# Kernel tuning notes

Measured on AMD Instinct MI355X. Metric: run time of the kernel, lower is better.

Reference implementation:

```python
import jax, jax.numpy as jnp
import numpy as np

BINS = np.array([1, 2, 3, 4, 8, 16, 32, 64], dtype=np.int32)


def setup_inputs() -> dict:
    N, G, F, H, K = 1024, 620, 20, 150, 128
    D_in = 3 * G + F  # 1880
    key = jax.random.key(0)
    ks = jax.random.split(key, 10)
    g = jax.random.normal(ks[0], (N, G), dtype=jnp.float32)
    si = jax.random.normal(ks[1], (N,), dtype=jnp.float32)
    i1 = jnp.sort(jax.random.randint(ks[2], (N,), 0, 8192)).astype(jnp.int32)
    i2 = jnp.sort(jax.random.randint(ks[3], (N,), 0, 8192)).astype(jnp.int32)
    dist_emb = jax.random.normal(ks[4], (9, F), dtype=jnp.float32) * 0.02
    W1 = jax.random.normal(ks[5], (D_in, H), dtype=jnp.float32) * (1.0 / np.sqrt(D_in))
    b1 = jnp.zeros((H,), jnp.float32)
    W2 = jax.random.normal(ks[6], (H, H), dtype=jnp.float32) * (1.0 / np.sqrt(H))
    b2 = jnp.zeros((H,), jnp.float32)
    W3 = jax.random.normal(ks[7], (H, 1), dtype=jnp.float32) * (1.0 / np.sqrt(H))
    b3 = jnp.zeros((1,), jnp.float32)
    return {"g": g, "si": si, "i1": i1, "i2": i2, "dist_emb": dist_emb,
            "W1": W1, "b1": b1, "W2": W2, "b2": b2, "W3": W3, "b3": b3, "K": K}


def reference(g, si, i1, i2, dist_emb, W1, b1, W2, b2, W3, b3, K):
    # Dropout is inference-disabled; epsilon dummy antecedent appended as last column.
    N, G = g.shape
    # span n's antecedents are spans [max(0, n-K), n); lay out as [N, K] window
    j_idx = jnp.arange(N)[:, None] - K + jnp.arange(K)[None, :]  # [N, K]
    valid = j_idx >= 0
    j = jnp.clip(j_idx, 0, N - 1)
    g_j = g[j]                      # [N, K, G] ragged gather (masked dense)
    g_i = g[:, None, :]             # [N, 1, G]
    # distance feature: bin(i.i2 - j.i1) with idx = #bins <= d
    d = i2[:, None] - i1[j]         # [N, K]
    bin_idx = jnp.searchsorted(jnp.asarray(BINS), d, side='right')
    de = dist_emb[bin_idx]          # [N, K, F]
    pairs = jnp.concatenate(
        [jnp.broadcast_to(g_i, (N, K, G)), g_j, g_i * g_j, de], axis=-1)  # [N, K, 3G+F]
    h = jax.nn.relu(jnp.einsum('nkd,dh->nkh', pairs, W1) + b1)
    h = jax.nn.relu(jnp.einsum('nkh,hm->nkm', h, W2) + b2)
    s = (jnp.einsum('nkh,ho->nko', h, W3) + b3)[..., 0]  # [N, K]
    sij = si[:, None] + si[j] + s
    sij = jnp.where(valid, sij, 0.0)
    eps = jnp.zeros((N, 1), sij.dtype)  # epsilon dummy score
    return jnp.concatenate([sij, eps], axis=-1)  # [N, K+1]
```

## Files before the change

kernel.cpp:

```cpp
#include <hip/hip_runtime.h>
#include <hip/hip_bf16.h>
#include <stdint.h>

typedef __attribute__((ext_vector_type(8))) short short8;
typedef __attribute__((ext_vector_type(4))) float float4_t;

#define N_PTS 1024
#define G_DIM 620
#define G_PAD 640
#define F_DIM 20
#define H_DIM 150
#define H_PAD 160
#define K_WIN 128
#define OUT_C (K_WIN + 1)

__device__ __forceinline__ float bf2f(short u) {
  union { unsigned int i; float f; } x;
  x.i = ((unsigned int)(unsigned short)u) << 16;
  return x.f;
}
__device__ __forceinline__ short f2bf(float f) {
  union { float f; unsigned int i; } x; x.f = f;
  unsigned int u = x.i;
  u += 0x7FFFu + ((u >> 16) & 1u);
  return (short)(u >> 16);
}
__device__ __forceinline__ short f2bf_hw(float f) {
  __hip_bfloat16 h = __float2bfloat16(f);
  union { __hip_bfloat16 h; short s; } u; u.h = h;
  return u.s;
}
__device__ __forceinline__ void gload_lds16(const void* g, void* l) {
  __builtin_amdgcn_global_load_lds(
      (const __attribute__((address_space(1))) unsigned int*)g,
      (__attribute__((address_space(3))) unsigned int*)l, 16, 0, 0);
}

__global__ void prep_pack(const float* __restrict__ g, const float* __restrict__ W1,
                          const float* __restrict__ W2, const float* __restrict__ dist_emb,
                          short* __restrict__ g_bf, short* __restrict__ W1cT,
                          short* __restrict__ W1abT, short* __restrict__ W2T,
                          float* __restrict__ deW) {
  __shared__ float lds[32 * 165];
  const int bx = blockIdx.x, tid = threadIdx.x;
  if (bx < 256) {
    const int n0 = bx * 4;
    for (int c = tid; c < 320; c += 256) {
      int r = c / 80, cc = c - r * 80;
      int n = n0 + r, d0 = cc * 8;
      short8 o;
      if (d0 + 8 <= G_DIM) {
        const float* src = g + n * G_DIM + d0;
        #pragma unroll
        for (int e = 0; e < 8; ++e) o[e] = f2bf(src[e]);
      } else {
        #pragma unroll
        for (int e = 0; e < 8; ++e) {
          int d = d0 + e;
          o[e] = (d < G_DIM) ? f2bf(g[n * G_DIM + d]) : (short)0;
        }
      }
      *(short8*)(g_bf + n * G_PAD + d0) = o;
    }
  } else if (bx < 316) {
    const int tb = bx - 256;
    const int third = tb / 20, dt = tb - third * 20;
    const int d0 = dt * 32;
    for (int c = tid; c < 1280; c += 256) {
      int dr = c / 40, ch4 = c - dr * 40;
      int dd = d0 + dr;
      int w1r = third * G_DIM + dd;
      #pragma unroll
      for (int e = 0; e < 4; ++e) {
        int h = ch4 * 4 + e;
        lds[dr * 165 + h] = (dd < G_DIM && h < H_DIM) ? W1[w1r * H_DIM + h] : 0.f;
      }
    }
    __syncthreads();
    short* outp = (third == 2) ? W1cT : (W1abT + third * H_PAD * G_PAD);
    for (int c = tid; c < 640; c += 256) {
      int h = c >> 2, ch = c & 3;
      short8 o;
      #pragma unroll
      for (int e = 0; e < 8; ++e) o[e] = f2bf(lds[(ch * 8 + e) * 165 + h]);
      *(short8*)(outp + h * G_PAD + d0 + ch * 8) = o;
    }
  } else if (bx < 320) {
    const int base = (bx - 316) * 6400;
    for (int c = tid; c < 6400; c += 256) {
      int q = base + c;
      int m = q / H_PAD, k = q - m * H_PAD;
      W2T[q] = (m < H_DIM && k < H_DIM) ? f2bf(W2[k * H_DIM + m]) : (short)0;
    }
  } else {
    for (int c = tid; c < 9 * H_PAD; c += 256) {
      int b = c / H_PAD, h = c - b * H_PAD;
      float acc = 0.f;
      if (h < H_DIM)
        for (int f = 0; f < F_DIM; ++f)
          acc += dist_emb[b * F_DIM + f] * W1[(3 * G_DIM + f) * H_DIM + h];
      deW[c] = acc;
    }
  }
}

__global__ __launch_bounds__(256) void prep_uv_mfma(
    const short* __restrict__ g_bf, const short* __restrict__ W1abT,
    const float* __restrict__ b1, float* __restrict__ U, float* __restrict__ V) {
  __shared__ __align__(16) char sA[32 * 128];
  __shared__ __align__(16) char sB[160 * 128];
  const int m0 = blockIdx.x * 32;
  const int yb = blockIdx.y * H_PAD;
  const int tid = threadIdx.x, lane = tid & 63, wid = tid >> 6;
  const int wm = wid >> 1, wn = wid & 1;
  const int lo4 = lane & 15, hi2 = lane >> 4;
  const int l8 = lane >> 3, c8 = lane & 7;
  const int xe = (c8 ^ (l8 & 7)) * 8;

  const float4_t fz = {0.f, 0.f, 0.f, 0.f};
  float4_t acc[5];
  #pragma unroll
  for (int b = 0; b < 5; ++b) acc[b] = fz;

  for (int step = 0; step < 10; ++step) {
    const int d0 = step * 64;
    {
      int row = wid * 8 + l8;
      gload_lds16(g_bf + (m0 + row) * G_PAD + d0 + xe, sA + (wid * 8) * 128);
    }
    #pragma unroll
    for (int cc = 0; cc < 5; ++cc) {
      int row = wid * 8 + cc * 32 + l8;
      gload_lds16(W1abT + (yb + row) * G_PAD + d0 + xe, sB + (wid * 8 + cc * 32) * 128);
    }
    __syncthreads();
    #pragma unroll
    for (int ks = 0; ks < 2; ++ks) {
      const int kb = ks * 64 + 16 * hi2;
      short8 af, bq[5];
      {
        int row = wm * 16 + lo4;
        af = *((const short8*)(sA + row * 128 + (kb ^ ((row & 7) << 4))));
      }
      #pragma unroll
      for (int nt = 0; nt < 5; ++nt) {
        int row = wn * 80 + nt * 16 + lo4;
        bq[nt] = *((const short8*)(sB + row * 128 + (kb ^ ((row & 7) << 4))));
      }
      #pragma unroll
      for (int nt = 0; nt < 5; ++nt)
        acc[nt] = __builtin_amdgcn_mfma_f32_16x16x32_bf16(af, bq[nt], acc[nt], 0, 0, 0);
    }
    __syncthreads();
  }

  const bool isU = (blockIdx.y == 0);
  float* O = isU ? U : V;
  #pragma unroll
  for (int r = 0; r < 4; ++r) {
    int m = m0 + wm * 16 + hi2 * 4 + r;
    #pragma unroll
    for (int nt = 0; nt < 5; ++nt) {
      int h = wn * 80 + nt * 16 + lo4;
      float v = acc[nt][r];
      if (h < H_DIM) { if (isU) v += b1[h]; } else { v = 0.f; }
      O[m * H_PAD + h] = v;
    }
  }
}

__global__ __launch_bounds__(256, 2) void pair_main(
    const short* __restrict__ g_bf, const short* __restrict__ W1cT,
    const short* __restrict__ W2T, const float* __restrict__ U,
    const float* __restrict__ V, const float* __restrict__ deW,
    const float* __restrict__ si, const int* __restrict__ i1,
    const int* __restrict__ i2, const float* __restrict__ W3,
    const float* __restrict__ b2, const float* __restrict__ b3,
    float* __restrict__ out) {
  __shared__ __align__(16) char smem[73728];
  __shared__ __align__(16) short gi_s[G_PAD];
  __shared__ float sj_s[K_WIN];
  __shared__ unsigned char bin_su[K_WIN];
  __shared__ float s_buf[2][K_WIN];

  char* const P0 = smem;
  char* const P1 = smem + 16384;
  char* const B0 = smem + 32768;
  char* const B1 = smem + 53248;
  char* const Hb = smem;

  const int bid = blockIdx.x;
  const int i = ((bid & 7) << 7) | (bid >> 3);
  const int tid = threadIdx.x;
  const int lane = tid & 63;
  const int wid = tid >> 6;
  const int wm = wid >> 1, wn = wid & 1;
  const int lo4 = lane & 15, hi2 = lane >> 4;
  const int l8 = lane >> 3, c8 = lane & 7;
  const int xe = (c8 ^ (l8 & 7)) * 8;
  const int tc8 = tid & 7;

  if (tid < G_PAD / 8)
    ((short8*)gi_s)[tid] = ((const short8*)(g_bf + i * G_PAD))[tid];
  if (tid < K_WIN) {
    int jr = i - K_WIN + tid, jc = jr < 0 ? 0 : jr;
    int d = i2[i] - i1[jc];
    bin_su[tid] = (unsigned char)((d >= 1) + (d >= 2) + (d >= 3) + (d >= 4) +
                                  (d >= 8) + (d >= 16) + (d >= 32) + (d >= 64));
    sj_s[tid] = si[jc];
  }
  __syncthreads();

  auto loadA = [&](int s, short8 (&gjv)[4], short8& gvv) {
    const int d0 = s * 64;
    gvv = *((const short8*)(gi_s + d0 + tc8 * 8));
    #pragma unroll
    for (int cc = 0; cc < 4; ++cc) {
      int c = tid + 256 * cc, row = c >> 3;
      int jr = i - K_WIN + row, jc = jr < 0 ? 0 : jr;
      gjv[cc] = *((const short8*)(g_bf + jc * G_PAD + d0 + tc8 * 8));
    }
  };
  auto stageB = [&](int s, char* B) {
    const int d0 = s * 64;
    #pragma unroll
    for (int cc = 0; cc < 5; ++cc) {
      int row = wid * 8 + cc * 32 + l8;
      gload_lds16(W1cT + row * G_PAD + d0 + xe, B + (wid * 8 + cc * 32) * 128);
    }
  };
  auto writeP = [&](char* P, const short8 (&gjv)[4], const short8& gvv) {
    #pragma unroll
    for (int cc = 0; cc < 4; ++cc) {
      int c = tid + 256 * cc, row = c >> 3;
      short8 p;
      #pragma unroll
      for (int e = 0; e < 8; ++e) p[e] = f2bf_hw(bf2f(gjv[cc][e]) * bf2f(gvv[e]));
      int byte = row * 128 + ((tc8 * 16) ^ ((row & 7) << 4));
      *((short8*)(P + byte)) = p;
    }
  };

  {
    short8 gjv[4], gvv;
    loadA(0, gjv, gvv);
    stageB(0, B0);
    writeP(P0, gjv, gvv);
  }

  const float4_t fz = {0.f, 0.f, 0.f, 0.f};
  float4_t acc[4][5];
  #pragma unroll
  for (int a = 0; a < 4; ++a)
    #pragma unroll
    for (int b = 0; b < 5; ++b) acc[a][b] = fz;

  for (int s = 0; s < 10; ++s) {
    char* Pc = (s & 1) ? P1 : P0;
    char* Bc = (s & 1) ? B1 : B0;
    char* Pn = (s & 1) ? P0 : P1;
    char* Bn = (s & 1) ? B0 : B1;
    __syncthreads();
    short8 gjv[4], gvv;
    if (s < 9) {
      loadA(s + 1, gjv, gvv);
      stageB(s + 1, Bn);
    }
    __builtin_amdgcn_s_setprio(1);
    #pragma unroll
    for (int ks = 0; ks < 2; ++ks) {
      const int kb = ks * 64 + 16 * hi2;
      short8 af[4], bq[5];
      #pragma unroll
      for (int mt = 0; mt < 4; ++mt) {
        int row = wm * 64 + mt * 16 + lo4;
        af[mt] = *((const short8*)(Pc + row * 128 + (kb ^ ((row & 7) << 4))));
      }
      #pragma unroll
      for (int nt = 0; nt < 5; ++nt) {
        int row = wn * 80 + nt * 16 + lo4;
        bq[nt] = *((const short8*)(Bc + row * 128 + (kb ^ ((row & 7) << 4))));
      }
      #pragma unroll
      for (int mt = 0; mt < 4; ++mt)
        #pragma unroll
        for (int nt = 0; nt < 5; ++nt)
          acc[mt][nt] = __builtin_amdgcn_mfma_f32_16x16x32_bf16(af[mt], bq[nt], acc[mt][nt], 0, 0, 0);
    }
    __builtin_amdgcn_s_setprio(0);
    if (s < 9) writeP(Pn, gjv, gvv);
  }
  __syncthreads();

  float uih[5];
  #pragma unroll
  for (int nt = 0; nt < 5; ++nt) uih[nt] = U[i * H_PAD + wn * 80 + nt * 16 + lo4];
  #pragma unroll
  for (int mt = 0; mt < 4; ++mt) {
    #pragma unroll
    for (int r = 0; r < 4; ++r) {
      int m = wm * 64 + mt * 16 + hi2 * 4 + r;
      int jr = i - K_WIN + m, jc = jr < 0 ? 0 : jr;
      const float* Vj = V + jc * H_PAD;
      const float* De = deW + bin_su[m] * H_PAD;
      #pragma unroll
      for (int nt = 0; nt < 5; ++nt) {
        int h = wn * 80 + nt * 16 + lo4;
        float val = acc[mt][nt][r] + uih[nt] + Vj[h] + De[h];
        val = (h < H_DIM) ? fmaxf(val, 0.f) : 0.f;
        int tile = h >> 6, hc = h & 63;
        int byte = tile * 16384 + m * 128 + ((hc * 2) ^ ((m & 7) << 4));
        *((short*)(Hb + byte)) = f2bf_hw(val);
      }
    }
  }
  {
    short8 z = {0, 0, 0, 0, 0, 0, 0, 0};
    for (int c = tid; c < 512; c += 256) {
      int row = c >> 2, cb = c & 3;
      int byte = 2 * 16384 + row * 128 + ((64 + cb * 16) ^ ((row & 7) << 4));
      *((short8*)(Hb + byte)) = z;
    }
  }
  __syncthreads();

  float4_t acc2[4][5];
  #pragma unroll
  for (int a = 0; a < 4; ++a)
    #pragma unroll
    for (int b = 0; b < 5; ++b) acc2[a][b] = fz;

  short8 bql[2][5];
  #pragma unroll
  for (int nt = 0; nt < 5; ++nt) {
    int row = wn * 80 + nt * 16 + lo4;
    bql[0][nt] = *(const short8*)(W2T + row * H_PAD + hi2 * 8);
  }
  #pragma unroll
  for (int ks = 0; ks < 5; ++ks) {
    const int cur = ks & 1;
    if (ks < 4) {
      #pragma unroll
      for (int nt = 0; nt < 5; ++nt) {
        int row = wn * 80 + nt * 16 + lo4;
        bql[cur ^ 1][nt] = *(const short8*)(W2T + row * H_PAD + (ks + 1) * 32 + hi2 * 8);
      }
    }
    short8 af[4];
    #pragma unroll
    for (int mt = 0; mt < 4; ++mt) {
      int row = wm * 64 + mt * 16 + lo4;
      int kb = (ks & 1) * 64 + hi2 * 16;
      af[mt] = *((const short8*)(Hb + (ks >> 1) * 16384 + row * 128 + (kb ^ ((row & 7) << 4))));
    }
    __builtin_amdgcn_s_setprio(1);
    #pragma unroll
    for (int mt = 0; mt < 4; ++mt)
      #pragma unroll
      for (int nt = 0; nt < 5; ++nt)
        acc2[mt][nt] = __builtin_amdgcn_mfma_f32_16x16x32_bf16(af[mt], bql[cur][nt], acc2[mt][nt], 0, 0, 0);
    __builtin_amdgcn_s_setprio(0);
  }

  float sp[4][4];
  #pragma unroll
  for (int mt = 0; mt < 4; ++mt)
    #pragma unroll
    for (int r = 0; r < 4; ++r) sp[mt][r] = 0.f;

  #pragma unroll
  for (int nt = 0; nt < 5; ++nt) {
    int h = wn * 80 + nt * 16 + lo4;
    float w3 = (h < H_DIM) ? W3[h] : 0.f;
    float bb = (h < H_DIM) ? b2[h] : 0.f;
    #pragma unroll
    for (int mt = 0; mt < 4; ++mt)
      #pragma unroll
      for (int r = 0; r < 4; ++r) {
        float hv = fmaxf(acc2[mt][nt][r] + bb, 0.f);
        sp[mt][r] += hv * w3;
      }
  }
  #pragma unroll
  for (int mt = 0; mt < 4; ++mt)
    #pragma unroll
    for (int r = 0; r < 4; ++r) {
      float v = sp[mt][r];
      v += __shfl_xor(v, 1);
      v += __shfl_xor(v, 2);
      v += __shfl_xor(v, 4);
      v += __shfl_xor(v, 8);
      sp[mt][r] = v;
    }
  if (lo4 == 0) {
    #pragma unroll
    for (int mt = 0; mt < 4; ++mt)
      #pragma unroll
      for (int r = 0; r < 4; ++r) {
        int m = wm * 64 + mt * 16 + hi2 * 4 + r;
        s_buf[wn][m] = sp[mt][r];
      }
  }
  __syncthreads();

  if (tid < K_WIN) {
    int m = tid;
    int jr = i - K_WIN + m;
    float sij = si[i] + sj_s[m] + s_buf[0][m] + s_buf[1][m] + b3[0];
    out[i * OUT_C + m] = (jr >= 0) ? sij : 0.f;
  }
  if (tid == K_WIN) out[i * OUT_C + K_WIN] = 0.f;
}

extern "C" void kernel_launch(void* const* d_in, const int* in_sizes, int n_in,
                              void* d_out, int out_size, void* d_ws, size_t ws_size,
                              hipStream_t stream) {
  const float* g  = (const float*)d_in[0];
  const float* si = (const float*)d_in[1];
  const int*   i1 = (const int*)d_in[2];
  const int*   i2 = (const int*)d_in[3];
  const float* de = (const float*)d_in[4];
  const float* W1 = (const float*)d_in[5];
  const float* b1 = (const float*)d_in[6];
  const float* W2 = (const float*)d_in[7];
  const float* b2 = (const float*)d_in[8];
  const float* W3 = (const float*)d_in[9];
  const float* b3 = (const float*)d_in[10];
  float* out = (float*)d_out;

  char* ws = (char*)d_ws;
  short* g_bf  = (short*)(ws);
  short* W1cT  = (short*)(ws + 1310720);
  short* W1abT = (short*)(ws + 1515520);
  short* W2T   = (short*)(ws + 1925120);
  float* U     = (float*)(ws + 1976320);
  float* V     = (float*)(ws + 2631680);
  float* deW   = (float*)(ws + 3287040);

  prep_pack<<<321, 256, 0, stream>>>(g, W1, W2, de, g_bf, W1cT, W1abT, W2T, deW);
  prep_uv_mfma<<<dim3(32, 2), 256, 0, stream>>>(g_bf, W1abT, b1, U, V);
  pair_main<<<N_PTS, 256, 0, stream>>>(g_bf, W1cT, W2T, U, V, deW,
                                       si, i1, i2, W3, b2, b3, out);
}
```

Baseline: 71.83 us.

## Prepack W1c into MFMA fragment layout and load B operands directly from global

Adds extra blocks to the U/V prep kernel that rearrange the W1c weight slice into per-lane MFMA fragment order. The main pair kernel then loads B fragments straight from global (L2) into registers instead of staging them through LDS, and shrinks shared memory from 72KB to 48KB. The K loop is manually unrolled by two with ping-pong register sets. This removes the LDS staging traffic and the LDS reads for B and could raise occupancy. In exchange it adds register pressure and relies on L2 latency being hidden for every block's weight reads.

Result: no change. 72.35 us (+0.7%).

```diff
diff --git a/kernel.cpp b/kernel.cpp
--- a/kernel.cpp
+++ b/kernel.cpp
@@ -106,7 +106,23 @@
 
 __global__ __launch_bounds__(256) void prep_uv_mfma(
     const short* __restrict__ g_bf, const short* __restrict__ W1abT,
-    const float* __restrict__ b1, float* __restrict__ U, float* __restrict__ V) {
+    const short* __restrict__ W1cT, const float* __restrict__ b1,
+    float* __restrict__ U, float* __restrict__ V, short* __restrict__ W1cF) {
+  if (blockIdx.x >= 32) {
+    const int s = (blockIdx.x - 32) + 5 * blockIdx.y;
+    const int tid = threadIdx.x;
+    #pragma unroll
+    for (int it = 0; it < 5; ++it) {
+      int slot = tid + 256 * it;
+      int lc = slot >> 6, lane = slot & 63;
+      int ks = lc / 10, wn = (lc / 5) & 1, nt = lc % 5;
+      int lo4 = lane & 15, hi2 = lane >> 4;
+      short8 v = *(const short8*)(W1cT + (wn * 80 + nt * 16 + lo4) * G_PAD +
+                                  s * 64 + ks * 32 + hi2 * 8);
+      *(short8*)(W1cF + (s * 20 + lc) * 512 + lane * 8) = v;
+    }
+    return;
+  }
   __shared__ __align__(16) char sA[32 * 128];
   __shared__ __align__(16) char sB[160 * 128];
   const int m0 = blockIdx.x * 32;
@@ -170,14 +186,14 @@
 }
 
 __global__ __launch_bounds__(256, 2) void pair_main(
-    const short* __restrict__ g_bf, const short* __restrict__ W1cT,
+    const short* __restrict__ g_bf, const short* __restrict__ W1cF,
     const short* __restrict__ W2T, const float* __restrict__ U,
     const float* __restrict__ V, const float* __restrict__ deW,
     const float* __restrict__ si, const int* __restrict__ i1,
     const int* __restrict__ i2, const float* __restrict__ W3,
     const float* __restrict__ b2, const float* __restrict__ b3,
     float* __restrict__ out) {
-  __shared__ __align__(16) char smem[73728];
+  __shared__ __align__(16) char smem[49152];
   __shared__ __align__(16) short gi_s[G_PAD];
   __shared__ float sj_s[K_WIN];
   __shared__ unsigned char bin_su[K_WIN];
@@ -185,8 +201,6 @@
 
   char* const P0 = smem;
   char* const P1 = smem + 16384;
-  char* const B0 = smem + 32768;
-  char* const B1 = smem + 53248;
   char* const Hb = smem;
 
   const int bid = blockIdx.x;
@@ -196,8 +210,6 @@
   const int wid = tid >> 6;
   const int wm = wid >> 1, wn = wid & 1;
   const int lo4 = lane & 15, hi2 = lane >> 4;
-  const int l8 = lane >> 3, c8 = lane & 7;
-  const int xe = (c8 ^ (l8 & 7)) * 8;
   const int tc8 = tid & 7;
 
   if (tid < G_PAD / 8)
@@ -211,6 +223,15 @@
   }
   __syncthreads();
 
+  const short8* const bfp = (const short8*)W1cF;
+
+  auto loadBq = [&](int s, short8 (&bq)[2][5]) {
+    #pragma unroll
+    for (int ks = 0; ks < 2; ++ks)
+      #pragma unroll
+      for (int nt = 0; nt < 5; ++nt)
+        bq[ks][nt] = bfp[(s * 20 + (ks * 2 + wn) * 5 + nt) * 64 + lane];
+  };
   auto loadA = [&](int s, short8 (&gjv)[4], short8& gvv) {
     const int d0 = s * 64;
     gvv = *((const short8*)(gi_s + d0 + tc8 * 8));
@@ -221,14 +242,6 @@
       gjv[cc] = *((const short8*)(g_bf + jc * G_PAD + d0 + tc8 * 8));
     }
   };
-  auto stageB = [&](int s, char* B) {
-    const int d0 = s * 64;
-    #pragma unroll
-    for (int cc = 0; cc < 5; ++cc) {
-      int row = wid * 8 + cc * 32 + l8;
-      gload_lds16(W1cT + row * G_PAD + d0 + xe, B + (wid * 8 + cc * 32) * 128);
-    }
-  };
   auto writeP = [&](char* P, const short8 (&gjv)[4], const short8& gvv) {
     #pragma unroll
     for (int cc = 0; cc < 4; ++cc) {
@@ -241,13 +254,6 @@
     }
   };
 
-  {
-    short8 gjv[4], gvv;
-    loadA(0, gjv, gvv);
-    stageB(0, B0);
-    writeP(P0, gjv, gvv);
-  }
-
   const float4_t fz = {0.f, 0.f, 0.f, 0.f};
   float4_t acc[4][5];
   #pragma unroll
@@ -255,40 +261,49 @@
     #pragma unroll
     for (int b = 0; b < 5; ++b) acc[a][b] = fz;
 
-  for (int s = 0; s < 10; ++s) {
-    char* Pc = (s & 1) ? P1 : P0;
-    char* Bc = (s & 1) ? B1 : B0;
-    char* Pn = (s & 1) ? P0 : P1;
-    char* Bn = (s & 1) ? B0 : B1;
-    __syncthreads();
-    short8 gjv[4], gvv;
-    if (s < 9) {
-      loadA(s + 1, gjv, gvv);
-      stageB(s + 1, Bn);
-    }
+  auto mfma_step = [&](const char* Pc, const short8 (&bq)[2][5]) {
     __builtin_amdgcn_s_setprio(1);
     #pragma unroll
     for (int ks = 0; ks < 2; ++ks) {
       const int kb = ks * 64 + 16 * hi2;
-      short8 af[4], bq[5];
+      short8 af[4];
       #pragma unroll
       for (int mt = 0; mt < 4; ++mt) {
         int row = wm * 64 + mt * 16 + lo4;
         af[mt] = *((const short8*)(Pc + row * 128 + (kb ^ ((row & 7) << 4))));
       }
       #pragma unroll
-      for (int nt = 0; nt < 5; ++nt) {
-        int row = wn * 80 + nt * 16 + lo4;
-        bq[nt] = *((const short8*)(Bc + row * 128 + (kb ^ ((row & 7) << 4))));
-      }
-      #pragma unroll
       for (int mt = 0; mt < 4; ++mt)
         #pragma unroll
         for (int nt = 0; nt < 5; ++nt)
-          acc[mt][nt] = __builtin_amdgcn_mfma_f32_16x16x32_bf16(af[mt], bq[nt], acc[mt][nt], 0, 0, 0);
+          acc[mt][nt] = __builtin_amdgcn_mfma_f32_16x16x32_bf16(af[mt], bq[ks][nt], acc[mt][nt], 0, 0, 0);
     }
     __builtin_amdgcn_s_setprio(0);
-    if (s < 9) writeP(Pn, gjv, gvv);
+  };
+
+  short8 gjv[4], gvv;
+  short8 bqE[2][5], bqO[2][5];
+  loadA(0, gjv, gvv);
+  loadBq(0, bqE);
+  writeP(P0, gjv, gvv);
+
+  #pragma unroll
+  for (int ss = 0; ss < 5; ++ss) {
+    const int s0 = 2 * ss;
+    __syncthreads();
+    loadA(s0 + 1, gjv, gvv);
+    loadBq(s0 + 1, bqO);
+    mfma_step(P0, bqE);
+    writeP(P1, gjv, gvv);
+    __syncthreads();
+    if (ss < 4) {
+      loadA(s0 + 2, gjv, gvv);
+      loadBq(s0 + 2, bqE);
+      mfma_step(P1, bqO);
+      writeP(P0, gjv, gvv);
+    } else {
+      mfma_step(P1, bqO);
+    }
   }
   __syncthreads();
 
@@ -436,9 +451,10 @@
   float* U     = (float*)(ws + 1976320);
   float* V     = (float*)(ws + 2631680);
   float* deW   = (float*)(ws + 3287040);
+  short* W1cF  = (short*)(ws + 3292800);
 
   prep_pack<<<321, 256, 0, stream>>>(g, W1, W2, de, g_bf, W1cT, W1abT, W2T, deW);
-  prep_uv_mfma<<<dim3(32, 2), 256, 0, stream>>>(g_bf, W1abT, b1, U, V);
-  pair_main<<<N_PTS, 256, 0, stream>>>(g_bf, W1cT, W2T, U, V, deW,
+  prep_uv_mfma<<<dim3(37, 2), 256, 0, stream>>>(g_bf, W1abT, W1cT, b1, U, V, W1cF);
+  pair_main<<<N_PTS, 256, 0, stream>>>(g_bf, W1cF, W2T, U, V, deW,
                                        si, i1, i2, W3, b2, b3, out);
 }
```
